# Kernel optimization log

Measured on AMD Instinct MI355X. Metric: run time of the kernel, lower is better.

Reference implementation:

```python
import jax, jax.numpy as jnp
import numpy as np

T, BS, N = 256, 512, 2048
FUDGE = 1e-4


def setup_inputs() -> dict:
    key = jax.random.key(0)
    ks = jax.random.split(key, 6)
    f32 = jnp.float32
    return {
        "noises": jax.random.normal(ks[0], (T, BS), f32) * 0.1,  # per-step process noise [T, bs]
        "ys": jax.random.normal(ks[1], (T,), f32),               # per-step scalar targets
        "qs": jax.random.normal(ks[2], (T,), f32),               # per-step scalar context input
        "z_biases": jax.random.normal(ks[3], (N,), f32),         # random-feature bias directions
        "w_in": jax.random.normal(ks[4], (N,), f32),             # random input weights
        "w_inq": jax.random.normal(ks[5], (N,), f32),            # random q-input weights
        # scalar learned params (legacy init values)
        "log_learning_rate": jnp.array(-6.0, f32),
        "log_learning_rate_decay": jnp.array(0.0, f32),
        "sigma_b": jnp.array(0.1, f32),
        "output_scale": jnp.array(1.0, f32),
        "u_feedback_scale": jnp.array(1.0, f32),
        "log_weight_decay": jnp.array(-0.001, f32),
        "q_scale": jnp.array(1.0, f32),
        "tauqlpf_m1": jnp.array(-1.0, f32),
        "tauylpf_m1": jnp.array(-1.0, f32),
    }


def _forward(noises, ys, qs, z_biases, w_in, w_inq,
             log_learning_rate, log_learning_rate_decay, sigma_b,
             output_scale, u_feedback_scale, log_weight_decay, q_scale,
             tauqlpf_m1, tauylpf_m1):
    bs = noises.shape[1]
    n = w_in.shape[0]
    softplus = lambda v: jnp.log1p(jnp.exp(v))
    biases = sigma_b * z_biases                    # [n]
    lr0 = jnp.exp(log_learning_rate)               # scalar
    tauq = 1.0 + softplus(tauqlpf_m1)
    tauy = 1.0 + softplus(tauylpf_m1)
    wd = jnp.exp(log_weight_decay)                 # tie_lr_weight_decay=False -> scalar decay
    lr_decay_rate = jnp.exp(log_learning_rate_decay)

    def step(carry, inp):
        w_out, u, e, lr_mult, qlp, ylp = carry
        y, noise_x, q = inp
        qlp = (1.0 - tauq) * qlp + tauq * q
        q_in = w_inq * (q_scale * qlp)             # [n]
        x = u * u_feedback_scale + e + noise_x     # noise injected at node 'x'; [bs]
        h = jax.nn.relu(biases[None, :] + x[:, None] * w_in[None, :] + q_in[None, :])  # [bs, n]
        u = jnp.einsum('kj,kj->k', w_out, h)       # [bs]
        a_mean = output_scale * u                  # [bs]
        # y observed every step (no None/NaN branch)
        ylp = (1.0 - tauy) * ylp + tauy * y
        e = ylp - u                                # [bs]
        lr = lr0 * lr_mult                         # [bs]
        dw = e[:, None] * h * lr[:, None]          # [bs, n]
        w_out = w_out + dw
        norms = jnp.sqrt(FUDGE + jnp.sum(dw * dw, axis=1))
        lr_mult = lr_mult * jnp.exp(-lr_decay_rate * norms)
        w_out = wd * w_out
        return (w_out, u, e, lr_mult, qlp, ylp), a_mean

    init = (jnp.zeros((bs, n), noises.dtype),
            jnp.zeros((bs,), noises.dtype),
            jnp.zeros((bs,), noises.dtype),
            jnp.ones((bs,), noises.dtype),
            jnp.zeros((), noises.dtype),
            jnp.zeros((), noises.dtype))
    _, a_means = jax.lax.scan(step, init, (ys, noises, qs))
    return a_means  # [T, bs]


def reference(noises, ys, qs, z_biases, w_in, w_inq,
              log_learning_rate, log_learning_rate_decay, sigma_b,
              output_scale, u_feedback_scale, log_weight_decay, q_scale,
              tauqlpf_m1, tauylpf_m1):
    return _forward(noises, ys, qs, z_biases, w_in, w_inq,
                    log_learning_rate, log_learning_rate_decay, sigma_b,
                    output_scale, u_feedback_scale, log_weight_decay, q_scale,
                    tauqlpf_m1, tauylpf_m1)
```

## Files before the change

### kernel.cpp

```cpp
#include <hip/hip_runtime.h>
#include <math.h>
#include <stdint.h>

#define T_STEPS 256
#define BS      512
#define N       2048
#define BLOCK   256
#define FUDGE   1e-4f

__global__ __launch_bounds__(BLOCK, 2)
void legacy_elbo_scan_kernel(
    const float* __restrict__ noises,
    const float* __restrict__ ys,
    const float* __restrict__ qs,
    const float* __restrict__ z_biases,
    const float* __restrict__ w_in,
    const float* __restrict__ w_inq,
    const float* __restrict__ p_llr,
    const float* __restrict__ p_llrd,
    const float* __restrict__ p_sigb,
    const float* __restrict__ p_oscale,
    const float* __restrict__ p_ufs,
    const float* __restrict__ p_lwd,
    const float* __restrict__ p_qscale,
    const float* __restrict__ p_tauq,
    const float* __restrict__ p_tauy,
    float* __restrict__ out)
{
    const int tid = threadIdx.x;
    const int blk = blockIdx.x;

    __shared__ float red_lds[16];
    if (tid < 16) red_lds[tid] = 0.0f;
    __syncthreads();

    const float sigb    = p_sigb[0];
    const float lr0     = expf(p_llr[0]);
    const float lr_decay= expf(p_llrd[0]);
    const float wd      = expf(p_lwd[0]);
    const float rwd     = 1.0f / wd;
    const float tauq    = 1.0f + log1pf(expf(p_tauq[0]));
    const float tauy    = 1.0f + log1pf(expf(p_tauy[0]));
    const float omtq    = 1.0f - tauq;
    const float omty    = 1.0f - tauy;
    const float qscale  = p_qscale[0];
    const float ufs     = p_ufs[0];
    const float oscale  = p_oscale[0];
    const float nld2    = -lr_decay * 1.4426950408889634f;

    const float* nzp = noises + blk;
    const int    ovo = blk * 4;

    asm volatile(
        "v_lshrrev_b32 v3, 6, %[vtid]\n\t"
        "v_lshlrev_b32 v4, 3, v3\n\t"
        "v_and_b32 v7, 63, %[vtid]\n\t"
        "v_cmp_eq_u32 vcc, 63, v7\n\t"
        "s_mov_b64 s[74:75], vcc\n\t"
        "v_cmp_eq_u32 vcc, 0, %[vtid]\n\t"
        "s_mov_b64 s[76:77], vcc\n\t"
        "v_mov_b32 v5, 0\n\t"
        "v_lshlrev_b32 v1, 4, %[vtid]\n\t"
        "v_add_u32 v2, 0x1000, v1\n\t"
        "global_load_dwordx4 v[40:43], v1, %[pzb]\n\t"
        "global_load_dwordx4 v[44:47], v2, %[pzb]\n\t"
        "global_load_dwordx4 v[48:51], v1, %[pwi]\n\t"
        "global_load_dwordx4 v[52:55], v2, %[pwi]\n\t"
        "global_load_dwordx4 v[56:59], v1, %[pwq]\n\t"
        "global_load_dwordx4 v[60:63], v2, %[pwq]\n\t"
        "s_waitcnt vmcnt(0)\n\t"
        "v_mul_f32 v40, %[osg], v40\n\t"  "v_mul_f32 v41, %[osg], v41\n\t"
        "v_mul_f32 v42, %[osg], v42\n\t"  "v_mul_f32 v43, %[osg], v43\n\t"
        "v_mul_f32 v44, %[osg], v44\n\t"  "v_mul_f32 v45, %[osg], v45\n\t"
        "v_mul_f32 v46, %[osg], v46\n\t"  "v_mul_f32 v47, %[osg], v47\n\t"
        "v_mov_b32 v64, 0\n\t" "v_mov_b32 v65, 0\n\t" "v_mov_b32 v66, 0\n\t" "v_mov_b32 v67, 0\n\t"
        "v_mov_b32 v68, 0\n\t" "v_mov_b32 v69, 0\n\t" "v_mov_b32 v70, 0\n\t" "v_mov_b32 v71, 0\n\t"
        "v_mov_b32 v20, 0\n\t" "v_mov_b32 v21, 0\n\t" "v_mov_b32 v22, 0\n\t" "v_mov_b32 v23, 0\n\t"
        "v_mov_b32 v24, 1.0\n\t" "v_mov_b32 v25, 1.0\n\t" "v_mov_b32 v26, 1.0\n\t"
        "v_mov_b32 v6, %[ovo]\n\t"
        "s_mov_b32 s60, 0\n\t"
        "s_mov_b32 s61, 0\n\t"
        "s_mov_b32 s62, 0\n\t"
        "s_load_dword s66, %[pys], s61\n\t"
        "s_load_dword s67, %[pqs], s61\n\t"
        "s_load_dword s68, %[pnz], s62\n\t"
        "s_waitcnt lgkmcnt(0)\n\t"
        "Lelbo2:\n\t"
        "s_add_u32 s63, s61, 4\n\t"
        "s_min_u32 s63, s63, 0x3fc\n\t"
        "s_add_u32 s64, s62, 0x800\n\t"
        "s_min_u32 s64, s64, 0x7f800\n\t"
        "s_load_dword s69, %[pys], s63\n\t"
        "s_load_dword s70, %[pqs], s63\n\t"
        "s_load_dword s71, %[pnz], s64\n\t"
        "v_mov_b32 v30, s67\n\t"
        "v_mul_f32 v20, %[omq], v20\n\t"
        "v_fmac_f32 v20, %[otq], v30\n\t"
        "v_mul_f32 v10, %[oq], v20\n\t"
        "v_mov_b32 v11, v10\n\t"
        "v_mov_b32 v8, s68\n\t"
        "v_add_f32 v8, v23, v8\n\t"
        "v_fmac_f32 v8, %[ouf], v22\n\t"
        "v_mov_b32 v9, v8\n\t"
        "v_mov_b32 v12, 0\n\t" "v_mov_b32 v13, 0\n\t"
        "v_mov_b32 v14, 0\n\t" "v_mov_b32 v15, 0\n\t"
        "v_pk_fma_f32 v[72:73], v[10:11], v[56:57], v[40:41]\n\t"
        "v_pk_fma_f32 v[74:75], v[10:11], v[58:59], v[42:43]\n\t"
        "v_pk_fma_f32 v[76:77], v[10:11], v[60:61], v[44:45]\n\t"
        "v_pk_fma_f32 v[78:79], v[10:11], v[62:63], v[46:47]\n\t"
        "v_pk_fma_f32 v[72:73], v[8:9], v[48:49], v[72:73]\n\t"
        "v_pk_fma_f32 v[74:75], v[8:9], v[50:51], v[74:75]\n\t"
        "v_pk_fma_f32 v[76:77], v[8:9], v[52:53], v[76:77]\n\t"
        "v_pk_fma_f32 v[78:79], v[8:9], v[54:55], v[78:79]\n\t"
        "v_max_f32 v72, 0, v72\n\t" "v_max_f32 v73, 0, v73\n\t"
        "v_max_f32 v74, 0, v74\n\t" "v_max_f32 v75, 0, v75\n\t"
        "v_max_f32 v76, 0, v76\n\t" "v_max_f32 v77, 0, v77\n\t"
        "v_max_f32 v78, 0, v78\n\t" "v_max_f32 v79, 0, v79\n\t"
        "v_pk_fma_f32 v[12:13], v[64:65], v[72:73], v[12:13]\n\t"
        "v_pk_fma_f32 v[14:15], v[72:73], v[72:73], v[14:15]\n\t"
        "v_pk_fma_f32 v[12:13], v[66:67], v[74:75], v[12:13]\n\t"
        "v_pk_fma_f32 v[14:15], v[74:75], v[74:75], v[14:15]\n\t"
        "v_pk_fma_f32 v[12:13], v[68:69], v[76:77], v[12:13]\n\t"
        "v_pk_fma_f32 v[14:15], v[76:77], v[76:77], v[14:15]\n\t"
        "v_pk_fma_f32 v[12:13], v[70:71], v[78:79], v[12:13]\n\t"
        "v_pk_fma_f32 v[14:15], v[78:79], v[78:79], v[14:15]\n\t"
        "v_add_f32 v12, v12, v13\n\t"
        "v_add_f32 v14, v14, v15\n\t"
        "s_nop 1\n\t"
        "v_mov_b32_dpp v30, v12 row_shr:1 row_mask:0xf bank_mask:0xf\n\t"
        "v_mov_b32_dpp v31, v14 row_shr:1 row_mask:0xf bank_mask:0xf\n\t"
        "v_add_f32 v12, v12, v30\n\t"
        "v_add_f32 v14, v14, v31\n\t"
        "s_nop 0\n\t"
        "v_mov_b32_dpp v30, v12 row_shr:2 row_mask:0xf bank_mask:0xf\n\t"
        "v_mov_b32_dpp v31, v14 row_shr:2 row_mask:0xf bank_mask:0xf\n\t"
        "v_add_f32 v12, v12, v30\n\t"
        "v_add_f32 v14, v14, v31\n\t"
        "s_nop 0\n\t"
        "v_mov_b32_dpp v30, v12 row_shr:4 row_mask:0xf bank_mask:0xf\n\t"
        "v_mov_b32_dpp v31, v14 row_shr:4 row_mask:0xf bank_mask:0xf\n\t"
        "v_add_f32 v12, v12, v30\n\t"
        "v_add_f32 v14, v14, v31\n\t"
        "s_nop 0\n\t"
        "v_mov_b32_dpp v30, v12 row_shr:8 row_mask:0xf bank_mask:0xf\n\t"
        "v_mov_b32_dpp v31, v14 row_shr:8 row_mask:0xf bank_mask:0xf\n\t"
        "v_add_f32 v12, v12, v30\n\t"
        "v_add_f32 v14, v14, v31\n\t"
        "s_nop 0\n\t"
        "v_mov_b32_dpp v30, v12 row_bcast:15 row_mask:0xf bank_mask:0xf\n\t"
        "v_mov_b32_dpp v31, v14 row_bcast:15 row_mask:0xf bank_mask:0xf\n\t"
        "v_add_f32 v12, v12, v30\n\t"
        "v_add_f32 v14, v14, v31\n\t"
        "s_nop 0\n\t"
        "v_mov_b32_dpp v30, v12 row_bcast:31 row_mask:0xf bank_mask:0xf\n\t"
        "v_mov_b32_dpp v31, v14 row_bcast:31 row_mask:0xf bank_mask:0xf\n\t"
        "v_add_f32 v12, v12, v30\n\t"
        "v_add_f32 v14, v14, v31\n\t"
        "s_nop 1\n\t"
        "s_and_saveexec_b64 s[72:73], s[74:75]\n\t"
        "ds_write2_b32 v4, v12, v14 offset0:0 offset1:1\n\t"
        "s_mov_b64 exec, s[72:73]\n\t"
        "s_waitcnt lgkmcnt(0)\n\t"
        "s_barrier\n\t"
        "ds_read_b128 v[32:35], v5\n\t"
        "ds_read_b128 v[36:39], v5 offset:16\n\t"
        "s_waitcnt lgkmcnt(0)\n\t"
        "v_pk_add_f32 v[32:33], v[32:33], v[34:35]\n\t"
        "v_pk_add_f32 v[36:37], v[36:37], v[38:39]\n\t"
        "v_pk_add_f32 v[32:33], v[32:33], v[36:37]\n\t"
        "v_mul_f32 v22, v25, v32\n\t"
        "v_mul_f32 v30, %[oos], v22\n\t"
        "s_and_saveexec_b64 s[72:73], s[76:77]\n\t"
        "global_store_dword v6, v30, %[pou]\n\t"
        "s_mov_b64 exec, s[72:73]\n\t"
        "v_add_u32 v6, 0x800, v6\n\t"
        "v_mov_b32 v30, s66\n\t"
        "v_mul_f32 v21, %[omy], v21\n\t"
        "v_fmac_f32 v21, %[oty], v30\n\t"
        "v_sub_f32 v23, v21, v22\n\t"
        "v_mul_f32 v27, %[olr], v23\n\t"
        "v_mul_f32 v27, v27, v24\n\t"
        "v_mul_f32 v28, v27, v26\n\t"
        "v_mov_b32 v29, v28\n\t"
        "v_pk_fma_f32 v[64:65], v[28:29], v[72:73], v[64:65]\n\t"
        "v_pk_fma_f32 v[66:67], v[28:29], v[74:75], v[66:67]\n\t"
        "v_pk_fma_f32 v[68:69], v[28:29], v[76:77], v[68:69]\n\t"
        "v_pk_fma_f32 v[70:71], v[28:29], v[78:79], v[70:71]\n\t"
        "v_mul_f32 v30, v27, v27\n\t"
        "v_mul_f32 v30, v33, v30\n\t"
        "v_add_f32 v30, 0x38d1b717, v30\n\t"
        "v_sqrt_f32 v30, v30\n\t"
        "s_nop 1\n\t"
        "v_mul_f32 v30, %[ond], v30\n\t"
        "v_exp_f32 v30, v30\n\t"
        "s_nop 1\n\t"
        "v_mul_f32 v24, v24, v30\n\t"
        "v_mul_f32 v25, %[owd], v25\n\t"
        "v_mul_f32 v26, %[orw], v26\n\t"
        "v_xor_b32 v4, 32, v4\n\t"
        "v_xor_b32 v5, 32, v5\n\t"
        "s_waitcnt lgkmcnt(0)\n\t"
        "s_mov_b32 s66, s69\n\t"
        "s_mov_b32 s67, s70\n\t"
        "s_mov_b32 s68, s71\n\t"
        "s_mov_b32 s61, s63\n\t"
        "s_mov_b32 s62, s64\n\t"
        "s_add_u32 s60, s60, 1\n\t"
        "s_cmp_lt_u32 s60, 0x100\n\t"
        "s_cbranch_scc1 Lelbo2\n\t"
        "s_waitcnt vmcnt(0)\n\t"
        :
        : [pys]"s"(ys), [pqs]"s"(qs), [pnz]"s"(nzp), [pou]"s"(out),
          [pzb]"s"(z_biases), [pwi]"s"(w_in), [pwq]"s"(w_inq),
          [vtid]"v"(tid), [ovo]"v"(ovo),
          [osg]"v"(sigb), [otq]"v"(tauq), [omq]"v"(omtq),
          [oty]"v"(tauy), [omy]"v"(omty), [oq]"v"(qscale),
          [ouf]"v"(ufs), [olr]"v"(lr0), [owd]"v"(wd), [orw]"v"(rwd),
          [oos]"v"(oscale), [ond]"v"(nld2)
        : "memory", "scc", "vcc",
          "s60","s61","s62","s63","s64","s65","s66","s67","s68","s69",
          "s70","s71","s72","s73","s74","s75","s76","s77",
          "v1","v2","v3","v4","v5","v6","v7","v8","v9","v10","v11",
          "v12","v13","v14","v15","v16","v17","v18","v19","v20","v21",
          "v22","v23","v24","v25","v26","v27","v28","v29","v30","v31",
          "v32","v33","v34","v35","v36","v37","v38","v39","v40","v41",
          "v42","v43","v44","v45","v46","v47","v48","v49","v50","v51",
          "v52","v53","v54","v55","v56","v57","v58","v59","v60","v61",
          "v62","v63","v64","v65","v66","v67","v68","v69","v70","v71",
          "v72","v73","v74","v75","v76","v77","v78","v79"
    );
}

extern "C" void kernel_launch(void* const* d_in, const int* in_sizes, int n_in,
                              void* d_out, int out_size, void* d_ws, size_t ws_size,
                              hipStream_t stream) {
    (void)in_sizes; (void)n_in; (void)d_ws; (void)ws_size; (void)out_size;
    const float* noises   = (const float*)d_in[0];
    const float* ys       = (const float*)d_in[1];
    const float* qs       = (const float*)d_in[2];
    const float* z_biases = (const float*)d_in[3];
    const float* w_in     = (const float*)d_in[4];
    const float* w_inq    = (const float*)d_in[5];
    const float* llr      = (const float*)d_in[6];
    const float* llrd     = (const float*)d_in[7];
    const float* sigb     = (const float*)d_in[8];
    const float* oscale   = (const float*)d_in[9];
    const float* ufs      = (const float*)d_in[10];
    const float* lwd      = (const float*)d_in[11];
    const float* qscale   = (const float*)d_in[12];
    const float* tauq     = (const float*)d_in[13];
    const float* tauy     = (const float*)d_in[14];
    float* out = (float*)d_out;

    hipLaunchKernelGGL(legacy_elbo_scan_kernel, dim3(BS), dim3(BLOCK), 64, stream,
                       noises, ys, qs, z_biases, w_in, w_inq,
                       llr, llrd, sigb, oscale, ufs, lwd, qscale, tauq, tauy,
                       out);
}
```

Baseline: 203.4 us.

## Software-pipeline scan loop: prefetch inputs via vector loads, overlap next-step precompute with barrier

Replaces per-step scalar loads of ys/qs/noise with a multi-step-deep vector-load prefetch ring. Moves the next step's q-term precompute and low-pass updates into the window between the LDS barrier and the reduction read. The per-thread dot-product and sum-of-squares chains become tree reductions over independent pk_mul/pk_add ops, and u*ufs+e is folded algebraically to y_lp + (ufs-1)*u. The goal is to shorten the serial critical path of each of the 256 dependent steps, at the cost of more VGPRs and rounding that differs slightly from before.

```diff
diff --git a/kernel.cpp b/kernel.cpp
--- a/kernel.cpp
+++ b/kernel.cpp
@@ -44,7 +44,7 @@
     const float omtq    = 1.0f - tauq;
     const float omty    = 1.0f - tauy;
     const float qscale  = p_qscale[0];
-    const float ufs     = p_ufs[0];
+    const float ufsm1   = p_ufs[0] - 1.0f;
     const float oscale  = p_oscale[0];
     const float nld2    = -lr_decay * 1.4426950408889634f;
 
@@ -57,7 +57,7 @@
         "v_and_b32 v7, 63, %[vtid]\n\t"
         "v_cmp_eq_u32 vcc, 63, v7\n\t"
         "s_mov_b64 s[74:75], vcc\n\t"
-        "v_cmp_eq_u32 vcc, 0, %[vtid]\n\t"
+        "v_cmp_eq_u32 vcc, 0, v7\n\t"
         "s_mov_b64 s[76:77], vcc\n\t"
         "v_mov_b32 v5, 0\n\t"
         "v_lshlrev_b32 v1, 4, %[vtid]\n\t"
@@ -68,6 +68,19 @@
         "global_load_dwordx4 v[52:55], v2, %[pwi]\n\t"
         "global_load_dwordx4 v[56:59], v1, %[pwq]\n\t"
         "global_load_dwordx4 v[60:63], v2, %[pwq]\n\t"
+        "v_mov_b32 v105, 0\n\t"
+        "v_mov_b32 v106, 0x1000\n\t"
+        "global_load_dword v96,  v105, %[pys]\n\t"
+        "global_load_dword v97,  v105, %[pqs]\n\t"
+        "global_load_dword v98,  v105, %[pnz]\n\t"
+        "global_load_dword v99,  v105, %[pys] offset:4\n\t"
+        "global_load_dword v100, v105, %[pqs] offset:4\n\t"
+        "global_load_dword v101, v105, %[pnz] offset:2048\n\t"
+        "global_load_dword v102, v105, %[pys] offset:8\n\t"
+        "global_load_dword v103, v105, %[pqs] offset:8\n\t"
+        "global_load_dword v104, v106, %[pnz]\n\t"
+        "v_mov_b32 v105, 12\n\t"
+        "v_mov_b32 v106, 0x1800\n\t"
         "s_waitcnt vmcnt(0)\n\t"
         "v_mul_f32 v40, %[osg], v40\n\t"  "v_mul_f32 v41, %[osg], v41\n\t"
         "v_mul_f32 v42, %[osg], v42\n\t"  "v_mul_f32 v43, %[osg], v43\n\t"
@@ -75,151 +88,150 @@
         "v_mul_f32 v46, %[osg], v46\n\t"  "v_mul_f32 v47, %[osg], v47\n\t"
         "v_mov_b32 v64, 0\n\t" "v_mov_b32 v65, 0\n\t" "v_mov_b32 v66, 0\n\t" "v_mov_b32 v67, 0\n\t"
         "v_mov_b32 v68, 0\n\t" "v_mov_b32 v69, 0\n\t" "v_mov_b32 v70, 0\n\t" "v_mov_b32 v71, 0\n\t"
-        "v_mov_b32 v20, 0\n\t" "v_mov_b32 v21, 0\n\t" "v_mov_b32 v22, 0\n\t" "v_mov_b32 v23, 0\n\t"
+        "v_mov_b32 v21, 0\n\t" "v_mov_b32 v22, 0\n\t"
         "v_mov_b32 v24, 1.0\n\t" "v_mov_b32 v25, 1.0\n\t" "v_mov_b32 v26, 1.0\n\t"
         "v_mov_b32 v6, %[ovo]\n\t"
-        "s_mov_b32 s60, 0\n\t"
-        "s_mov_b32 s61, 0\n\t"
-        "s_mov_b32 s62, 0\n\t"
-        "s_load_dword s66, %[pys], s61\n\t"
-        "s_load_dword s67, %[pqs], s61\n\t"
-        "s_load_dword s68, %[pnz], s62\n\t"
-        "s_waitcnt lgkmcnt(0)\n\t"
-        "Lelbo2:\n\t"
-        "s_add_u32 s63, s61, 4\n\t"
-        "s_min_u32 s63, s63, 0x3fc\n\t"
-        "s_add_u32 s64, s62, 0x800\n\t"
-        "s_min_u32 s64, s64, 0x7f800\n\t"
-        "s_load_dword s69, %[pys], s63\n\t"
-        "s_load_dword s70, %[pqs], s63\n\t"
-        "s_load_dword s71, %[pnz], s64\n\t"
-        "v_mov_b32 v30, s67\n\t"
-        "v_mul_f32 v20, %[omq], v20\n\t"
-        "v_fmac_f32 v20, %[otq], v30\n\t"
+        "v_mul_f32 v20, %[otq], v97\n\t"
         "v_mul_f32 v10, %[oq], v20\n\t"
         "v_mov_b32 v11, v10\n\t"
-        "v_mov_b32 v8, s68\n\t"
-        "v_add_f32 v8, v23, v8\n\t"
-        "v_fmac_f32 v8, %[ouf], v22\n\t"
+        "v_pk_fma_f32 v[80:81], v[10:11], v[56:57], v[40:41]\n\t"
+        "v_pk_fma_f32 v[82:83], v[10:11], v[58:59], v[42:43]\n\t"
+        "v_pk_fma_f32 v[84:85], v[10:11], v[60:61], v[44:45]\n\t"
+        "v_pk_fma_f32 v[86:87], v[10:11], v[62:63], v[46:47]\n\t"
+        "v_mov_b32 v8, v98\n\t"
         "v_mov_b32 v9, v8\n\t"
-        "v_mov_b32 v12, 0\n\t" "v_mov_b32 v13, 0\n\t"
-        "v_mov_b32 v14, 0\n\t" "v_mov_b32 v15, 0\n\t"
-        "v_pk_fma_f32 v[72:73], v[10:11], v[56:57], v[40:41]\n\t"
-        "v_pk_fma_f32 v[74:75], v[10:11], v[58:59], v[42:43]\n\t"
-        "v_pk_fma_f32 v[76:77], v[10:11], v[60:61], v[44:45]\n\t"
-        "v_pk_fma_f32 v[78:79], v[10:11], v[62:63], v[46:47]\n\t"
-        "v_pk_fma_f32 v[72:73], v[8:9], v[48:49], v[72:73]\n\t"
-        "v_pk_fma_f32 v[74:75], v[8:9], v[50:51], v[74:75]\n\t"
-        "v_pk_fma_f32 v[76:77], v[8:9], v[52:53], v[76:77]\n\t"
-        "v_pk_fma_f32 v[78:79], v[8:9], v[54:55], v[78:79]\n\t"
+        "v_mov_b32 v27, %[olr]\n\t"
+        "s_mov_b32 s60, 0\n\t"
+        "Lelbo4:\n\t"
+        "v_pk_fma_f32 v[72:73], v[8:9], v[48:49], v[80:81]\n\t"
+        "v_pk_fma_f32 v[74:75], v[8:9], v[50:51], v[82:83]\n\t"
+        "v_pk_fma_f32 v[76:77], v[8:9], v[52:53], v[84:85]\n\t"
+        "v_pk_fma_f32 v[78:79], v[8:9], v[54:55], v[86:87]\n\t"
         "v_max_f32 v72, 0, v72\n\t" "v_max_f32 v73, 0, v73\n\t"
         "v_max_f32 v74, 0, v74\n\t" "v_max_f32 v75, 0, v75\n\t"
         "v_max_f32 v76, 0, v76\n\t" "v_max_f32 v77, 0, v77\n\t"
         "v_max_f32 v78, 0, v78\n\t" "v_max_f32 v79, 0, v79\n\t"
-        "v_pk_fma_f32 v[12:13], v[64:65], v[72:73], v[12:13]\n\t"
-        "v_pk_fma_f32 v[14:15], v[72:73], v[72:73], v[14:15]\n\t"
-        "v_pk_fma_f32 v[12:13], v[66:67], v[74:75], v[12:13]\n\t"
-        "v_pk_fma_f32 v[14:15], v[74:75], v[74:75], v[14:15]\n\t"
-        "v_pk_fma_f32 v[12:13], v[68:69], v[76:77], v[12:13]\n\t"
-        "v_pk_fma_f32 v[14:15], v[76:77], v[76:77], v[14:15]\n\t"
-        "v_pk_fma_f32 v[12:13], v[70:71], v[78:79], v[12:13]\n\t"
-        "v_pk_fma_f32 v[14:15], v[78:79], v[78:79], v[14:15]\n\t"
+        "v_pk_mul_f32 v[12:13], v[64:65], v[72:73]\n\t"
+        "v_pk_mul_f32 v[14:15], v[66:67], v[74:75]\n\t"
+        "v_pk_mul_f32 v[16:17], v[68:69], v[76:77]\n\t"
+        "v_pk_mul_f32 v[18:19], v[70:71], v[78:79]\n\t"
+        "v_pk_mul_f32 v[88:89], v[72:73], v[72:73]\n\t"
+        "v_pk_mul_f32 v[90:91], v[74:75], v[74:75]\n\t"
+        "v_pk_mul_f32 v[92:93], v[76:77], v[76:77]\n\t"
+        "v_pk_mul_f32 v[94:95], v[78:79], v[78:79]\n\t"
+        "v_pk_add_f32 v[12:13], v[12:13], v[14:15]\n\t"
+        "v_pk_add_f32 v[16:17], v[16:17], v[18:19]\n\t"
+        "v_pk_add_f32 v[88:89], v[88:89], v[90:91]\n\t"
+        "v_pk_add_f32 v[92:93], v[92:93], v[94:95]\n\t"
+        "v_pk_add_f32 v[12:13], v[12:13], v[16:17]\n\t"
+        "v_pk_add_f32 v[88:89], v[88:89], v[92:93]\n\t"
         "v_add_f32 v12, v12, v13\n\t"
-        "v_add_f32 v14, v14, v15\n\t"
+        "v_add_f32 v16, v88, v89\n\t"
         "s_nop 1\n\t"
         "v_mov_b32_dpp v30, v12 row_shr:1 row_mask:0xf bank_mask:0xf\n\t"
-        "v_mov_b32_dpp v31, v14 row_shr:1 row_mask:0xf bank_mask:0xf\n\t"
-        "v_add_f32 v12, v12, v30\n\t"
-        "v_add_f32 v14, v14, v31\n\t"
+        "v_mov_b32_dpp v31, v16 row_shr:1 row_mask:0xf bank_mask:0xf\n\t"
+        "v_add_f32 v12, v12, v30\n\t"
+        "v_add_f32 v16, v16, v31\n\t"
         "s_nop 0\n\t"
         "v_mov_b32_dpp v30, v12 row_shr:2 row_mask:0xf bank_mask:0xf\n\t"
-        "v_mov_b32_dpp v31, v14 row_shr:2 row_mask:0xf bank_mask:0xf\n\t"
-        "v_add_f32 v12, v12, v30\n\t"
-        "v_add_f32 v14, v14, v31\n\t"
+        "v_mov_b32_dpp v31, v16 row_shr:2 row_mask:0xf bank_mask:0xf\n\t"
+        "v_add_f32 v12, v12, v30\n\t"
+        "v_add_f32 v16, v16, v31\n\t"
         "s_nop 0\n\t"
         "v_mov_b32_dpp v30, v12 row_shr:4 row_mask:0xf bank_mask:0xf\n\t"
-        "v_mov_b32_dpp v31, v14 row_shr:4 row_mask:0xf bank_mask:0xf\n\t"
-        "v_add_f32 v12, v12, v30\n\t"
-        "v_add_f32 v14, v14, v31\n\t"
+        "v_mov_b32_dpp v31, v16 row_shr:4 row_mask:0xf bank_mask:0xf\n\t"
+        "v_add_f32 v12, v12, v30\n\t"
+        "v_add_f32 v16, v16, v31\n\t"
         "s_nop 0\n\t"
         "v_mov_b32_dpp v30, v12 row_shr:8 row_mask:0xf bank_mask:0xf\n\t"
-        "v_mov_b32_dpp v31, v14 row_shr:8 row_mask:0xf bank_mask:0xf\n\t"
-        "v_add_f32 v12, v12, v30\n\t"
-        "v_add_f32 v14, v14, v31\n\t"
+        "v_mov_b32_dpp v31, v16 row_shr:8 row_mask:0xf bank_mask:0xf\n\t"
+        "v_add_f32 v12, v12, v30\n\t"
+        "v_add_f32 v16, v16, v31\n\t"
         "s_nop 0\n\t"
         "v_mov_b32_dpp v30, v12 row_bcast:15 row_mask:0xf bank_mask:0xf\n\t"
-        "v_mov_b32_dpp v31, v14 row_bcast:15 row_mask:0xf bank_mask:0xf\n\t"
-        "v_add_f32 v12, v12, v30\n\t"
-        "v_add_f32 v14, v14, v31\n\t"
+        "v_mov_b32_dpp v31, v16 row_bcast:15 row_mask:0xf bank_mask:0xf\n\t"
+        "v_add_f32 v12, v12, v30\n\t"
+        "v_add_f32 v16, v16, v31\n\t"
         "s_nop 0\n\t"
         "v_mov_b32_dpp v30, v12 row_bcast:31 row_mask:0xf bank_mask:0xf\n\t"
-        "v_mov_b32_dpp v31, v14 row_bcast:31 row_mask:0xf bank_mask:0xf\n\t"
-        "v_add_f32 v12, v12, v30\n\t"
-        "v_add_f32 v14, v14, v31\n\t"
+        "v_mov_b32_dpp v31, v16 row_bcast:31 row_mask:0xf bank_mask:0xf\n\t"
+        "v_add_f32 v12, v12, v30\n\t"
+        "v_add_f32 v16, v16, v31\n\t"
         "s_nop 1\n\t"
         "s_and_saveexec_b64 s[72:73], s[74:75]\n\t"
-        "ds_write2_b32 v4, v12, v14 offset0:0 offset1:1\n\t"
+        "ds_write2_b32 v4, v12, v16 offset0:0 offset1:1\n\t"
         "s_mov_b64 exec, s[72:73]\n\t"
         "s_waitcnt lgkmcnt(0)\n\t"
         "s_barrier\n\t"
         "ds_read_b128 v[32:35], v5\n\t"
         "ds_read_b128 v[36:39], v5 offset:16\n\t"
+        "v_mul_f32 v20, %[omq], v20\n\t"
+        "v_fmac_f32 v20, %[otq], v100\n\t"
+        "v_mul_f32 v10, %[oq], v20\n\t"
+        "v_mov_b32 v11, v10\n\t"
+        "v_pk_fma_f32 v[80:81], v[10:11], v[56:57], v[40:41]\n\t"
+        "v_pk_fma_f32 v[82:83], v[10:11], v[58:59], v[42:43]\n\t"
+        "v_pk_fma_f32 v[84:85], v[10:11], v[60:61], v[44:45]\n\t"
+        "v_pk_fma_f32 v[86:87], v[10:11], v[62:63], v[46:47]\n\t"
+        "v_mul_f32 v21, %[omy], v21\n\t"
+        "v_fmac_f32 v21, %[oty], v96\n\t"
+        "v_add_f32 v1, v21, v101\n\t"
+        "v_mul_f32 v27, %[olr], v24\n\t"
+        "v_xor_b32 v4, 32, v4\n\t"
+        "v_xor_b32 v5, 32, v5\n\t"
+        "s_add_u32 s60, s60, 1\n\t"
         "s_waitcnt lgkmcnt(0)\n\t"
         "v_pk_add_f32 v[32:33], v[32:33], v[34:35]\n\t"
         "v_pk_add_f32 v[36:37], v[36:37], v[38:39]\n\t"
         "v_pk_add_f32 v[32:33], v[32:33], v[36:37]\n\t"
         "v_mul_f32 v22, v25, v32\n\t"
+        "v_fma_f32 v8, %[oum], v22, v1\n\t"
+        "v_mov_b32 v9, v8\n\t"
         "v_mul_f32 v30, %[oos], v22\n\t"
         "s_and_saveexec_b64 s[72:73], s[76:77]\n\t"
         "global_store_dword v6, v30, %[pou]\n\t"
         "s_mov_b64 exec, s[72:73]\n\t"
         "v_add_u32 v6, 0x800, v6\n\t"
-        "v_mov_b32 v30, s66\n\t"
-        "v_mul_f32 v21, %[omy], v21\n\t"
-        "v_fmac_f32 v21, %[oty], v30\n\t"
         "v_sub_f32 v23, v21, v22\n\t"
-        "v_mul_f32 v27, %[olr], v23\n\t"
-        "v_mul_f32 v27, v27, v24\n\t"
-        "v_mul_f32 v28, v27, v26\n\t"
+        "v_mul_f32 v31, v27, v23\n\t"
+        "v_mul_f32 v28, v31, v26\n\t"
         "v_mov_b32 v29, v28\n\t"
+        "v_mul_f32 v30, v31, v31\n\t"
+        "v_mul_f32 v30, v33, v30\n\t"
+        "v_add_f32 v30, 0x38d1b717, v30\n\t"
+        "v_sqrt_f32 v30, v30\n\t"
         "v_pk_fma_f32 v[64:65], v[28:29], v[72:73], v[64:65]\n\t"
         "v_pk_fma_f32 v[66:67], v[28:29], v[74:75], v[66:67]\n\t"
         "v_pk_fma_f32 v[68:69], v[28:29], v[76:77], v[68:69]\n\t"
         "v_pk_fma_f32 v[70:71], v[28:29], v[78:79], v[70:71]\n\t"
-        "v_mul_f32 v30, v27, v27\n\t"
-        "v_mul_f32 v30, v33, v30\n\t"
-        "v_add_f32 v30, 0x38d1b717, v30\n\t"
-        "v_sqrt_f32 v30, v30\n\t"
-        "s_nop 1\n\t"
         "v_mul_f32 v30, %[ond], v30\n\t"
         "v_exp_f32 v30, v30\n\t"
-        "s_nop 1\n\t"
-        "v_mul_f32 v24, v24, v30\n\t"
+        "s_waitcnt vmcnt(1)\n\t"
+        "v_mov_b32 v96, v99\n\t"  "v_mov_b32 v97, v100\n\t" "v_mov_b32 v98, v101\n\t"
+        "v_mov_b32 v99, v102\n\t" "v_mov_b32 v100, v103\n\t" "v_mov_b32 v101, v104\n\t"
+        "global_load_dword v102, v105, %[pys]\n\t"
+        "global_load_dword v103, v105, %[pqs]\n\t"
+        "global_load_dword v104, v106, %[pnz]\n\t"
+        "v_add_u32 v105, 4, v105\n\t"
+        "v_min_u32 v105, 0x3fc, v105\n\t"
+        "v_add_u32 v106, 0x800, v106\n\t"
+        "v_min_u32 v106, 0x7f800, v106\n\t"
         "v_mul_f32 v25, %[owd], v25\n\t"
         "v_mul_f32 v26, %[orw], v26\n\t"
-        "v_xor_b32 v4, 32, v4\n\t"
-        "v_xor_b32 v5, 32, v5\n\t"
-        "s_waitcnt lgkmcnt(0)\n\t"
-        "s_mov_b32 s66, s69\n\t"
-        "s_mov_b32 s67, s70\n\t"
-        "s_mov_b32 s68, s71\n\t"
-        "s_mov_b32 s61, s63\n\t"
-        "s_mov_b32 s62, s64\n\t"
-        "s_add_u32 s60, s60, 1\n\t"
+        "v_mul_f32 v24, v24, v30\n\t"
         "s_cmp_lt_u32 s60, 0x100\n\t"
-        "s_cbranch_scc1 Lelbo2\n\t"
-        "s_waitcnt vmcnt(0)\n\t"
+        "s_cbranch_scc1 Lelbo4\n\t"
+        "s_waitcnt vmcnt(0) lgkmcnt(0)\n\t"
         :
         : [pys]"s"(ys), [pqs]"s"(qs), [pnz]"s"(nzp), [pou]"s"(out),
           [pzb]"s"(z_biases), [pwi]"s"(w_in), [pwq]"s"(w_inq),
           [vtid]"v"(tid), [ovo]"v"(ovo),
           [osg]"v"(sigb), [otq]"v"(tauq), [omq]"v"(omtq),
           [oty]"v"(tauy), [omy]"v"(omty), [oq]"v"(qscale),
-          [ouf]"v"(ufs), [olr]"v"(lr0), [owd]"v"(wd), [orw]"v"(rwd),
+          [oum]"v"(ufsm1), [olr]"v"(lr0), [owd]"v"(wd), [orw]"v"(rwd),
           [oos]"v"(oscale), [ond]"v"(nld2)
         : "memory", "scc", "vcc",
-          "s60","s61","s62","s63","s64","s65","s66","s67","s68","s69",
-          "s70","s71","s72","s73","s74","s75","s76","s77",
+          "s60","s72","s73","s74","s75","s76","s77",
           "v1","v2","v3","v4","v5","v6","v7","v8","v9","v10","v11",
           "v12","v13","v14","v15","v16","v17","v18","v19","v20","v21",
           "v22","v23","v24","v25","v26","v27","v28","v29","v30","v31",
@@ -227,7 +239,10 @@
           "v42","v43","v44","v45","v46","v47","v48","v49","v50","v51",
           "v52","v53","v54","v55","v56","v57","v58","v59","v60","v61",
           "v62","v63","v64","v65","v66","v67","v68","v69","v70","v71",
-          "v72","v73","v74","v75","v76","v77","v78","v79"
+          "v72","v73","v74","v75","v76","v77","v78","v79","v80","v81",
+          "v82","v83","v84","v85","v86","v87","v88","v89","v90","v91",
+          "v92","v93","v94","v95","v96","v97","v98","v99","v100","v101",
+          "v102","v103","v104","v105","v106"
     );
 }
 
```

Result: no change. 201.5 us (-0.9%).
